# Kernel optimization log

Hardware: AMD Instinct MI355X
Metric: run time of the kernel (lower is better)

Reference implementation:

```python
import jax, jax.numpy as jnp
import numpy as np

B, M, C, D, FF, FEAT = 1, 1024, 128, 512, 1024, 20
PAIR = 3 * D + 2 * FEAT  # slow_scorer_size = 1576


def _ffnn(x, W0, b0, W1, b1):
    # FFNN(depth=1): hidden relu layer then linear output (eval mode, no dropout)
    return jax.nn.relu(x @ W0 + b0) @ W1 + b1


def _batch_gather(x, idx):
    # x: [B, M, ...], idx: [B, ...] int -> gather along mention dim per batch
    return jax.vmap(lambda xb, ib: xb[ib])(x, idx)


def _bucket_distance(d):
    # log-scale distance buckets 0..9 (identity for d<=4)
    log_idx = jnp.floor(jnp.log(jnp.maximum(d, 1).astype(jnp.float32)) / jnp.log(2.0)).astype(jnp.int32) + 3
    return jnp.clip(jnp.where(d <= 4, d, log_idx), 0, 9)


def setup_inputs() -> dict:
    key = jax.random.key(0)
    ks = jax.random.split(key, 10)
    s = 0.02
    return {
        'mention_emb': jax.random.normal(ks[0], (B, M, D), dtype=jnp.float32),
        'mention_cluster_ids': jax.random.randint(ks[1], (B, M), 0, 200),
        'mention_speaker_ids': jax.random.randint(ks[2], (B, M), 0, 2),
        'ms_W0': jax.random.normal(ks[3], (D, FF), dtype=jnp.float32) * s,
        'ms_b0': jnp.zeros((FF,), jnp.float32),
        'ms_W1': jax.random.normal(ks[4], (FF, 1), dtype=jnp.float32) * s,
        'ms_b1': jnp.zeros((1,), jnp.float32),
        'sp_W0': jax.random.normal(ks[5], (PAIR, FF), dtype=jnp.float32) * s,
        'sp_b0': jnp.zeros((FF,), jnp.float32),
        'sp_W1': jax.random.normal(ks[6], (FF, 1), dtype=jnp.float32) * s,
        'sp_b1': jnp.zeros((1,), jnp.float32),
        'speaker_emb': jax.random.normal(ks[7], (2, FEAT), dtype=jnp.float32) * s,
        'bucket_emb': jax.random.normal(ks[8], (10, FEAT), dtype=jnp.float32) * s,
    }


def reference(mention_emb, mention_cluster_ids, mention_speaker_ids,
              ms_W0, ms_b0, ms_W1, ms_b1,
              sp_W0, sp_b0, sp_W1, sp_b1,
              speaker_emb, bucket_emb):
    # mention scoring
    mention_scores = _ffnn(mention_emb, ms_W0, ms_b0, ms_W1, ms_b1)[..., 0]  # [B, M]

    # get_antecedent_info: fixed window of C previous mentions
    offsets = jnp.arange(1, C + 1)[None, None, :]                    # [1,1,C]
    raw = jnp.arange(M)[None, :, None] - offsets                      # [1,M,C]
    antecedents = jnp.broadcast_to(jnp.clip(raw, 0, M - 1), (B, M, C))
    ant_mask = jnp.broadcast_to(raw >= 0, (B, M, C))

    fast_scores = _batch_gather(mention_scores, antecedents) + mention_scores[:, :, None]
    antecedent_emb = _batch_gather(mention_emb, antecedents)          # [B,M,C,D]

    # slow pair scorer features
    same_speaker = (_batch_gather(mention_speaker_ids, antecedents) == mention_speaker_ids[:, :, None]).astype(jnp.int32)
    speaker_feat = speaker_emb[same_speaker]                          # [B,M,C,FEAT]
    bucket_feat = jnp.broadcast_to(bucket_emb[_bucket_distance(offsets)], (B, M, C, FEAT))

    src = jnp.broadcast_to(mention_emb[:, :, None, :], (B, M, C, D))
    pair_emb = jnp.concatenate([src, antecedent_emb, src * antecedent_emb, speaker_feat, bucket_feat], axis=-1)
    slow_scores = _ffnn(pair_emb, sp_W0, sp_b0, sp_W1, sp_b1)[..., 0]  # [B,M,C]

    antecedent_scores = fast_scores + slow_scores + jnp.log(ant_mask.astype(jnp.float32))
    overall_scores = jnp.concatenate([jnp.zeros((B, M, 1), jnp.float32), antecedent_scores], axis=2)
    overall_dist = jax.nn.softmax(overall_scores, axis=-1)
    eps = 1e-6
    overall_dist = jnp.clip(overall_dist, eps, 1.0 - eps)
    overall_dist = overall_dist / jnp.sum(overall_dist, axis=-1, keepdims=True)

    # coref loss from cluster ids
    ant_cluster = _batch_gather(mention_cluster_ids, antecedents) * ant_mask.astype(mention_cluster_ids.dtype)
    same_cluster = ant_cluster == mention_cluster_ids[:, :, None]
    non_dummy = (mention_cluster_ids > 0)[:, :, None]
    ant_labels = same_cluster & non_dummy
    dummy_labels = ~jnp.any(ant_labels, axis=2, keepdims=True)
    overall_labels = jnp.concatenate([dummy_labels, ant_labels], axis=2)
    loss = -jnp.sum(jnp.log(overall_dist) * overall_labels.astype(jnp.float32), axis=2)
    loss = jnp.mean(jnp.sum(loss, axis=1))
    return overall_dist, loss
```

## Files before the change

kernel.cpp:

```cpp
#include <hip/hip_runtime.h>
#include <math.h>

#define MM 1024
#define DD 512
#define CC 128
#define LDSR 516


typedef __attribute__((ext_vector_type(8))) short bf16x8;
typedef __attribute__((ext_vector_type(4), aligned(8))) short bf16x4a;
typedef __attribute__((ext_vector_type(4))) float f32x4;

__device__ __forceinline__ ushort bf16_rn(float x) {
    uint u = __float_as_uint(x);
    uint r = u + 0x7fffu + ((u >> 16) & 1u);
    return (ushort)(r >> 16);
}
__device__ __forceinline__ float bf16_to_f(ushort u) {
    return __uint_as_float(((uint)u) << 16);
}
__device__ __forceinline__ bf16x8 ld_lds16(const ushort* p) {
    bf16x4a lo = *(const bf16x4a*)p;
    bf16x4a hi = *(const bf16x4a*)(p + 4);
    return __builtin_shufflevector(lo, hi, 0, 1, 2, 3, 4, 5, 6, 7);
}

__global__ __launch_bounds__(256) void prep_emb(const float* __restrict__ emb,
                                                ushort* __restrict__ embb)
{
    int i = blockIdx.x * 256 + threadIdx.x;
    float2 v = ((const float2*)emb)[i];
    ushort2 o;
    o.x = bf16_rn(v.x);
    o.y = bf16_rn(v.y);
    ((ushort2*)embb)[i] = o;
}

__global__ __launch_bounds__(256) void prep_wall(const float* __restrict__ ms_W0,
                                                 const float* __restrict__ sp_W0,
                                                 ushort* __restrict__ Wall)
{
    __shared__ float t[64][65];
    const int k0 = blockIdx.x * 64;
    const int n0 = blockIdx.y * 64;
    const int g = n0 >> 10;
    const float* src = (g == 0) ? ms_W0 : (sp_W0 + (size_t)(g - 1) * 512 * 1024);
    const int col0 = n0 & 1023;
    const int tr = threadIdx.x >> 6, tc = threadIdx.x & 63;
#pragma unroll
    for (int i = 0; i < 16; ++i) {
        int k = tr + i * 4;
        t[k][tc] = src[(size_t)(k0 + k) * 1024 + col0 + tc];
    }
    __syncthreads();
    const int f = threadIdx.x >> 2;
    const int c4 = threadIdx.x & 3;
    ushort tmp[16];
#pragma unroll
    for (int j = 0; j < 16; ++j) tmp[j] = bf16_rn(t[c4 * 16 + j][f]);
    uint4* dst = (uint4*)(Wall + (size_t)(n0 + f) * 512 + k0 + c4 * 16);
    dst[0] = *(uint4*)&tmp[0];
    dst[1] = *(uint4*)&tmp[8];
}

__global__ __launch_bounds__(64) void prep_wfragP(const float* __restrict__ W,
                                                  ushort* __restrict__ dst_frag)
{
    const int bid = blockIdx.x;
    const int l = threadIdx.x;
    const int g2 = bid >> 5, s = (bid >> 1) & 15, j = bid & 1;
    const int wave = g2 >> 2, ft = g2 & 3;
    const int t16 = wave * 8 + ft * 2 + j;
    const int f = t16 * 16 + (l & 15);
    const int kb = s * 32 + ((l >> 4) & 3) * 8;
    ushort tmp[8];
#pragma unroll
    for (int e = 0; e < 8; ++e) tmp[e] = bf16_rn(W[(size_t)(kb + e) * 1024 + f]);
    uint4* dst = (uint4*)(dst_frag + (size_t)bid * 512 + l * 8);
    *dst = *(uint4*)&tmp[0];
}

__global__ __launch_bounds__(256) void gemm_h_mfma(
    const ushort* __restrict__ embb, const ushort* __restrict__ Wall,
    float* __restrict__ H)
{
    const int n0 = blockIdx.x * 128;
    const int m0 = blockIdx.y * 128;
    const int lane = threadIdx.x & 63, wave = threadIdx.x >> 6;
    const int wx = wave & 1, wy = wave >> 1;
    const int l15 = lane & 15, lq = lane >> 4;

    const ushort* arow[4];
#pragma unroll
    for (int mi = 0; mi < 4; ++mi)
        arow[mi] = embb + (size_t)(m0 + wy * 64 + mi * 16 + l15) * 512;
    const ushort* brow[4];
#pragma unroll
    for (int ni = 0; ni < 4; ++ni)
        brow[ni] = Wall + (size_t)(n0 + wx * 64 + ni * 16 + l15) * 512;

    f32x4 acc[4][4];
#pragma unroll
    for (int i = 0; i < 4; ++i)
#pragma unroll
        for (int j = 0; j < 4; ++j) acc[i][j] = (f32x4)0.f;

    for (int kt = 0; kt < 512; kt += 32) {
        const int ko = kt + lq * 8;
        bf16x8 av[4], bv[4];
#pragma unroll
        for (int mi = 0; mi < 4; ++mi) av[mi] = *(const bf16x8*)(arow[mi] + ko);
#pragma unroll
        for (int ni = 0; ni < 4; ++ni) bv[ni] = *(const bf16x8*)(brow[ni] + ko);
#pragma unroll
        for (int mi = 0; mi < 4; ++mi)
#pragma unroll
            for (int ni = 0; ni < 4; ++ni)
                acc[mi][ni] = __builtin_amdgcn_mfma_f32_16x16x32_bf16(av[mi], bv[ni], acc[mi][ni], 0, 0, 0);
    }
#pragma unroll
    for (int mi = 0; mi < 4; ++mi)
#pragma unroll
        for (int r = 0; r < 4; ++r) {
            int mrow = m0 + wy * 64 + mi * 16 + lq * 4 + r;
#pragma unroll
            for (int ni = 0; ni < 4; ++ni)
                H[(size_t)mrow * 3072 + n0 + wx * 64 + ni * 16 + l15] = acc[mi][ni][r];
        }
}

__global__ void small_proj(const float* __restrict__ speaker_emb,
                           const float* __restrict__ bucket_emb,
                           const float* __restrict__ sp_W0,
                           float* __restrict__ spk_proj, float* __restrict__ bkt_proj)
{
    int r = blockIdx.x;
    const float* e; const float* W; float* out;
    if (r < 2) { e = speaker_emb + r * 20; W = sp_W0 + (size_t)1536 * 1024; out = spk_proj + r * 1024; }
    else       { e = bucket_emb + (r - 2) * 20; W = sp_W0 + (size_t)1556 * 1024; out = bkt_proj + (r - 2) * 1024; }
    float ek[20];
#pragma unroll
    for (int k = 0; k < 20; ++k) ek[k] = e[k];
    for (int f = threadIdx.x; f < 1024; f += blockDim.x) {
        float s = 0.f;
#pragma unroll
        for (int k = 0; k < 20; ++k) s = fmaf(ek[k], W[(size_t)k * 1024 + f], s);
        out[f] = s;
    }
}

__global__ __launch_bounds__(256) void mention_score(
    const float* __restrict__ H, const float* __restrict__ ms_b0,
    const float* __restrict__ ms_W1, const float* __restrict__ ms_b1,
    float* __restrict__ ms)
{
    int m = blockIdx.x;
    float v = 0.f;
    for (int f = threadIdx.x; f < 1024; f += 256) {
        float h = H[(size_t)m * 3072 + f] + ms_b0[f];
        v += fmaxf(h, 0.f) * ms_W1[f];
    }
#pragma unroll
    for (int o = 1; o < 64; o <<= 1) v += __shfl_xor(v, o);
    __shared__ float sm[4];
    if ((threadIdx.x & 63) == 0) sm[threadIdx.x >> 6] = v;
    __syncthreads();
    if (threadIdx.x == 0) ms[m] = sm[0] + sm[1] + sm[2] + sm[3] + ms_b1[0];
}

__global__ __launch_bounds__(512, 8) void pair_mfma(
    const ushort* __restrict__ embb, const ushort* __restrict__ WfragP,
    const float* __restrict__ H, const float* __restrict__ spk_proj,
    const float* __restrict__ bkt_proj, const float* __restrict__ sp_b0,
    const float* __restrict__ sp_W1, const int* __restrict__ speaker,
    float* __restrict__ slow)
{
    extern __shared__ ushort Alds[];
    float* red = (float*)(Alds + 32 * LDSR);
    int* meta_ss = (int*)(red + 8 * 32);
    int* meta_bk = meta_ss + 32;
    const int m = blockIdx.x;
    const int cq = blockIdx.y;
    const int cbase = cq * 32;
    const int tid = threadIdx.x;
    const int spk_m = speaker[m];

    {
        const int c = tid & 31;
        const int kh = (tid >> 5) * 32;
        int a = m - 1 - (cbase + c); if (a < 0) a = 0;
        const ushort* ea = embb + (size_t)a * 512 + kh;
        const ushort* em = embb + (size_t)m * 512 + kh;
        ushort* dst = Alds + c * LDSR + kh;
#pragma unroll
        for (int j = 0; j < 32; j += 8) {
            bf16x8 va = *(const bf16x8*)(ea + j);
            bf16x8 vm = *(const bf16x8*)(em + j);
            uint pr[4];
#pragma unroll
            for (int p = 0; p < 4; ++p) {
                float q0 = bf16_to_f((ushort)va[2 * p])     * bf16_to_f((ushort)vm[2 * p]);
                float q1 = bf16_to_f((ushort)va[2 * p + 1]) * bf16_to_f((ushort)vm[2 * p + 1]);
                pr[p] = __builtin_amdgcn_perm(__float_as_uint(q1), __float_as_uint(q0), 0x07060302u);
            }
            *(uint2*)(dst + j)     = *(uint2*)&pr[0];
            *(uint2*)(dst + j + 4) = *(uint2*)&pr[2];
        }
        if (tid < 32) {
            meta_ss[c] = (speaker[a] == spk_m) ? 1 : 0;
            int off = cbase + c + 1;
            int bk;
            if (off <= 4) bk = off;
            else { bk = 31 - __clz(off) + 3; if (bk > 9) bk = 9; }
            meta_bk[c] = bk;
        }
    }
    __syncthreads();

    const int lane = tid & 63;
    const int wave = __builtin_amdgcn_readfirstlane(tid >> 6);
    const int l15 = lane & 15, lq = lane >> 4;
    const ushort* ab0 = Alds + l15 * LDSR + lq * 8;

    const float* Hsrc = H + m * 3072 + 1024;
    const float* Hant = H + 2048;

    float sacc[2][4];
#pragma unroll
    for (int ct = 0; ct < 2; ++ct)
#pragma unroll
        for (int r = 0; r < 4; ++r) sacc[ct][r] = 0.f;

#pragma unroll 1
    for (int ft = 0; ft < 4; ++ft) {
        const int f0a = wave * 128 + ft * 32;
        const ushort* bb = WfragP + (size_t)(wave * 4 + ft) * 16384 + (size_t)lane * 8;
        f32x4 acc[2][2];
#pragma unroll
        for (int i = 0; i < 2; ++i)
#pragma unroll
            for (int j = 0; j < 2; ++j) acc[i][j] = (f32x4)0.f;

#pragma unroll 4
        for (int s = 0; s < 16; ++s) {
            bf16x8 b0 = *(const bf16x8*)(bb + s * 1024);
            bf16x8 b1 = *(const bf16x8*)(bb + s * 1024 + 512);
            bf16x8 a0 = ld_lds16(ab0 + s * 32);
            bf16x8 a1 = ld_lds16(ab0 + 16 * LDSR + s * 32);
            __builtin_amdgcn_s_setprio(1);
            acc[0][0] = __builtin_amdgcn_mfma_f32_16x16x32_bf16(a0, b0, acc[0][0], 0, 0, 0);
            acc[0][1] = __builtin_amdgcn_mfma_f32_16x16x32_bf16(a0, b1, acc[0][1], 0, 0, 0);
            acc[1][0] = __builtin_amdgcn_mfma_f32_16x16x32_bf16(a1, b0, acc[1][0], 0, 0, 0);
            acc[1][1] = __builtin_amdgcn_mfma_f32_16x16x32_bf16(a1, b1, acc[1][1], 0, 0, 0);
            __builtin_amdgcn_s_setprio(0);
        }

        float srcb[2], w1v[2], sp0v[2], sp1v[2];
#pragma unroll
        for (int fi = 0; fi < 2; ++fi) {
            const int fcol = f0a + fi * 16 + l15;
            srcb[fi] = Hsrc[fcol] + sp_b0[fcol];
            w1v[fi]  = sp_W1[fcol];
            sp0v[fi] = spk_proj[fcol];
            sp1v[fi] = spk_proj[1024 + fcol];
        }
#pragma unroll
        for (int ct = 0; ct < 2; ++ct) {
#pragma unroll
            for (int reg = 0; reg < 4; ++reg) {
                const int cl = ct * 16 + lq * 4 + reg;
                int a = m - 1 - (cbase + cl); if (a < 0) a = 0;
                const int ss = meta_ss[cl];
                const int aidx = a * 3072;
                const int bidx = meta_bk[cl] << 10;
                float s = sacc[ct][reg];
#pragma unroll
                for (int fi = 0; fi < 2; ++fi) {
                    const int fcol = f0a + fi * 16 + l15;
                    float bval = bkt_proj[bidx + fcol];
                    float pre = acc[ct][fi][reg] + srcb[fi] + Hant[aidx + fcol]
                              + (ss ? sp1v[fi] : sp0v[fi]) + bval;
                    s += fmaxf(pre, 0.f) * w1v[fi];
                }
                sacc[ct][reg] = s;
            }
        }
    }

#pragma unroll
    for (int ct = 0; ct < 2; ++ct) {
#pragma unroll
        for (int reg = 0; reg < 4; ++reg) {
            float s = sacc[ct][reg];
            s += __shfl_xor(s, 1); s += __shfl_xor(s, 2);
            s += __shfl_xor(s, 4); s += __shfl_xor(s, 8);
            if (l15 == 0) red[wave * 32 + ct * 16 + lq * 4 + reg] = s;
        }
    }
    __syncthreads();
    if (tid < 32) {
        float s = 0.f;
#pragma unroll
        for (int i = 0; i < 8; ++i) s += red[i * 32 + tid];
        slow[m * 128 + cbase + tid] = s;
    }
}

__device__ __forceinline__ float bsum2(float v, float* sm) {
#pragma unroll
    for (int o = 1; o < 64; o <<= 1) v += __shfl_xor(v, o);
    __syncthreads();
    if ((threadIdx.x & 63) == 0) sm[threadIdx.x >> 6] = v;
    __syncthreads();
    return sm[0] + sm[1];
}
__device__ __forceinline__ float bmax2(float v, float* sm) {
#pragma unroll
    for (int o = 1; o < 64; o <<= 1) v = fmaxf(v, __shfl_xor(v, o));
    __syncthreads();
    if ((threadIdx.x & 63) == 0) sm[threadIdx.x >> 6] = v;
    __syncthreads();
    return fmaxf(sm[0], sm[1]);
}

__global__ __launch_bounds__(128) void softmax_loss(
    const float* __restrict__ slow, const float* __restrict__ ms,
    const float* __restrict__ sp_b1, const int* __restrict__ cluster,
    float* __restrict__ out, float* __restrict__ loss_partial)
{
    const int m = blockIdx.x, c = threadIdx.x;
    __shared__ float sm[2];
    const int raw = m - 1 - c;
    const bool maskv = raw >= 0;
    const int a = maskv ? raw : 0;
    float score = slow[(size_t)m * 128 + c] + sp_b1[0] + ms[m] + ms[a];
    if (!maskv) score = -INFINITY;

    float mx = fmaxf(bmax2(score, sm), 0.f);
    float e = expf(score - mx);
    float e0 = expf(0.f - mx);
    float sum = bsum2(e, sm) + e0;
    float p = e / sum, p0 = e0 / sum;
    const float eps = 1e-6f;
    p  = fminf(fmaxf(p,  eps), 1.f - eps);
    p0 = fminf(fmaxf(p0, eps), 1.f - eps);
    float sum2 = bsum2(p, sm) + p0;
    p /= sum2; p0 /= sum2;
    out[(size_t)m * 129 + 1 + c] = p;
    if (c == 0) out[(size_t)m * 129] = p0;

    const int cid = cluster[m];
    const bool lbl = maskv && (cid > 0) && (cluster[a] == cid);
    float anyc = bsum2(lbl ? 1.f : 0.f, sm);
    float lsum = bsum2(lbl ? -logf(p) : 0.f, sm);
    if (c == 0) {
        if (anyc == 0.f) lsum += -logf(p0);
        loss_partial[m] = lsum;
    }
}

__global__ void loss_sum(const float* __restrict__ lp, float* __restrict__ out) {
    float v = 0.f;
    for (int i = threadIdx.x; i < 1024; i += 256) v += lp[i];
#pragma unroll
    for (int o = 1; o < 64; o <<= 1) v += __shfl_xor(v, o);
    __shared__ float sm[4];
    if ((threadIdx.x & 63) == 0) sm[threadIdx.x >> 6] = v;
    __syncthreads();
    if (threadIdx.x == 0) out[(size_t)1024 * 129] = sm[0] + sm[1] + sm[2] + sm[3];
}

extern "C" void kernel_launch(void* const* d_in, const int* in_sizes, int n_in,
                              void* d_out, int out_size, void* d_ws, size_t ws_size,
                              hipStream_t stream)
{
    const float* emb   = (const float*)d_in[0];
    const int*   clus  = (const int*)  d_in[1];
    const int*   spk   = (const int*)  d_in[2];
    const float* ms_W0 = (const float*)d_in[3];
    const float* ms_b0 = (const float*)d_in[4];
    const float* ms_W1 = (const float*)d_in[5];
    const float* ms_b1 = (const float*)d_in[6];
    const float* sp_W0 = (const float*)d_in[7];
    const float* sp_b0 = (const float*)d_in[8];
    const float* sp_W1 = (const float*)d_in[9];
    const float* sp_b1 = (const float*)d_in[10];
    const float* spke  = (const float*)d_in[11];
    const float* bkte  = (const float*)d_in[12];

    float* ws = (float*)d_ws;
    float* H        = ws;
    float* slow     = ws + 3145728;
    float* spk_proj = ws + 3276800;
    float* bkt_proj = ws + 3278848;
    float* msc      = ws + 3289088;
    float* lossp    = ws + 3290112;
    ushort* embb    = (ushort*)(ws + 3291136);
    ushort* Wall    = (ushort*)(ws + 3553280);
    ushort* WfragP  = Wall + (size_t)3072 * 512;
    float* out = (float*)d_out;

    const int pair_lds = 32 * LDSR * 2 + 8 * 32 * 4 + 2 * 32 * 4;

    static bool attr_set = false;
    if (!attr_set) {
        hipFuncSetAttribute((const void*)&pair_mfma,
                            hipFuncAttributeMaxDynamicSharedMemorySize,
                            pair_lds);
        attr_set = true;
    }

    hipLaunchKernelGGL(prep_emb, dim3(1024), dim3(256), 0, stream, emb, embb);
    hipLaunchKernelGGL(prep_wall, dim3(8, 48), dim3(256), 0, stream, ms_W0, sp_W0, Wall);
    hipLaunchKernelGGL(prep_wfragP, dim3(1024), dim3(64), 0, stream,
                       sp_W0 + (size_t)1024 * 1024, WfragP);
    hipLaunchKernelGGL(gemm_h_mfma, dim3(24, 8), dim3(256), 0, stream, embb, Wall, H);
    hipLaunchKernelGGL(small_proj, dim3(12), dim3(256), 0, stream, spke, bkte, sp_W0, spk_proj, bkt_proj);
    hipLaunchKernelGGL(mention_score, dim3(1024), dim3(256), 0, stream, H, ms_b0, ms_W1, ms_b1, msc);
    hipLaunchKernelGGL(pair_mfma, dim3(1024, 4), dim3(512), pair_lds, stream,
                       embb, WfragP, H, spk_proj, bkt_proj, sp_b0, sp_W1, spk, slow);
    hipLaunchKernelGGL(softmax_loss, dim3(1024), dim3(128), 0, stream,
                       slow, msc, sp_b1, clus, out, lossp);
    hipLaunchKernelGGL(loss_sum, dim3(1), dim3(256), 0, stream, lossp, out);
}
```

Baseline: 347.9 us.

## Merge prep kernels into one launch and fuse mention scoring into GEMM epilogue

The four preprocessing kernels (emb cast, W transpose, fragment pack, small projections) become one kernel that dispatches on block index. Mention scoring is folded into the H GEMM epilogue: blocks covering the first 1024 columns apply bias, relu and the W1 dot product, then atomically add into the mention scores instead of writing H. The intent is fewer launches and no write-then-reread of that part of H. In exchange it adds a memset, float atomics that make summation order nondeterministic, and moves ms_b1 into softmax as 2*ms_b1.

```diff
diff --git a/kernel.cpp b/kernel.cpp
--- a/kernel.cpp
+++ b/kernel.cpp
@@ -25,64 +25,88 @@
     return __builtin_shufflevector(lo, hi, 0, 1, 2, 3, 4, 5, 6, 7);
 }
 
-__global__ __launch_bounds__(256) void prep_emb(const float* __restrict__ emb,
-                                                ushort* __restrict__ embb)
-{
-    int i = blockIdx.x * 256 + threadIdx.x;
-    float2 v = ((const float2*)emb)[i];
-    ushort2 o;
-    o.x = bf16_rn(v.x);
-    o.y = bf16_rn(v.y);
-    ((ushort2*)embb)[i] = o;
-}
-
-__global__ __launch_bounds__(256) void prep_wall(const float* __restrict__ ms_W0,
-                                                 const float* __restrict__ sp_W0,
-                                                 ushort* __restrict__ Wall)
-{
-    __shared__ float t[64][65];
-    const int k0 = blockIdx.x * 64;
-    const int n0 = blockIdx.y * 64;
-    const int g = n0 >> 10;
-    const float* src = (g == 0) ? ms_W0 : (sp_W0 + (size_t)(g - 1) * 512 * 1024);
-    const int col0 = n0 & 1023;
-    const int tr = threadIdx.x >> 6, tc = threadIdx.x & 63;
-#pragma unroll
-    for (int i = 0; i < 16; ++i) {
-        int k = tr + i * 4;
-        t[k][tc] = src[(size_t)(k0 + k) * 1024 + col0 + tc];
-    }
-    __syncthreads();
-    const int f = threadIdx.x >> 2;
-    const int c4 = threadIdx.x & 3;
-    ushort tmp[16];
-#pragma unroll
-    for (int j = 0; j < 16; ++j) tmp[j] = bf16_rn(t[c4 * 16 + j][f]);
-    uint4* dst = (uint4*)(Wall + (size_t)(n0 + f) * 512 + k0 + c4 * 16);
-    dst[0] = *(uint4*)&tmp[0];
-    dst[1] = *(uint4*)&tmp[8];
-}
-
-__global__ __launch_bounds__(64) void prep_wfragP(const float* __restrict__ W,
-                                                  ushort* __restrict__ dst_frag)
+__global__ __launch_bounds__(256) void prep_all(
+    const float* __restrict__ emb, ushort* __restrict__ embb,
+    const float* __restrict__ ms_W0, const float* __restrict__ sp_W0,
+    ushort* __restrict__ Wall, ushort* __restrict__ WfragP,
+    const float* __restrict__ speaker_emb, const float* __restrict__ bucket_emb,
+    float* __restrict__ spk_proj, float* __restrict__ bkt_proj)
 {
     const int bid = blockIdx.x;
-    const int l = threadIdx.x;
-    const int g2 = bid >> 5, s = (bid >> 1) & 15, j = bid & 1;
-    const int wave = g2 >> 2, ft = g2 & 3;
-    const int t16 = wave * 8 + ft * 2 + j;
-    const int f = t16 * 16 + (l & 15);
-    const int kb = s * 32 + ((l >> 4) & 3) * 8;
-    ushort tmp[8];
-#pragma unroll
-    for (int e = 0; e < 8; ++e) tmp[e] = bf16_rn(W[(size_t)(kb + e) * 1024 + f]);
-    uint4* dst = (uint4*)(dst_frag + (size_t)bid * 512 + l * 8);
-    *dst = *(uint4*)&tmp[0];
-}
-
-__global__ __launch_bounds__(256) void gemm_h_mfma(
+    const int tid = threadIdx.x;
+
+    if (bid < 1024) {
+        int i = bid * 256 + tid;
+        float2 v = ((const float2*)emb)[i];
+        ushort2 o;
+        o.x = bf16_rn(v.x);
+        o.y = bf16_rn(v.y);
+        ((ushort2*)embb)[i] = o;
+        return;
+    }
+    if (bid < 1408) {
+        __shared__ float t[64][65];
+        const int r = bid - 1024;
+        const int k0 = (r & 7) * 64;
+        const int n0 = (r >> 3) * 64;
+        const int g = n0 >> 10;
+        const float* src = (g == 0) ? ms_W0 : (sp_W0 + (size_t)(g - 1) * 512 * 1024);
+        const int col0 = n0 & 1023;
+        const int tr = tid >> 6, tc = tid & 63;
+#pragma unroll
+        for (int i = 0; i < 16; ++i) {
+            int k = tr + i * 4;
+            t[k][tc] = src[(size_t)(k0 + k) * 1024 + col0 + tc];
+        }
+        __syncthreads();
+        const int f = tid >> 2;
+        const int c4 = tid & 3;
+        ushort tmp[16];
+#pragma unroll
+        for (int j = 0; j < 16; ++j) tmp[j] = bf16_rn(t[c4 * 16 + j][f]);
+        uint4* dst = (uint4*)(Wall + (size_t)(n0 + f) * 512 + k0 + c4 * 16);
+        dst[0] = *(uint4*)&tmp[0];
+        dst[1] = *(uint4*)&tmp[8];
+        return;
+    }
+    if (bid < 1664) {
+        const int b4 = (bid - 1408) * 4 + (tid >> 6);
+        const int l = tid & 63;
+        const int g2 = b4 >> 5, s = (b4 >> 1) & 15, j = b4 & 1;
+        const int wv = g2 >> 2, ft = g2 & 3;
+        const int t16 = wv * 8 + ft * 2 + j;
+        const int f = t16 * 16 + (l & 15);
+        const int kb = s * 32 + ((l >> 4) & 3) * 8;
+        const float* W = sp_W0 + (size_t)1024 * 1024;
+        ushort tmp[8];
+#pragma unroll
+        for (int e = 0; e < 8; ++e) tmp[e] = bf16_rn(W[(size_t)(kb + e) * 1024 + f]);
+        uint4* dst = (uint4*)(WfragP + (size_t)b4 * 512 + l * 8);
+        *dst = *(uint4*)&tmp[0];
+        return;
+    }
+    {
+        const int r = bid - 1664;
+        const float* e; const float* W; float* out;
+        if (r < 2) { e = speaker_emb + r * 20; W = sp_W0 + (size_t)1536 * 1024; out = spk_proj + r * 1024; }
+        else       { e = bucket_emb + (r - 2) * 20; W = sp_W0 + (size_t)1556 * 1024; out = bkt_proj + (r - 2) * 1024; }
+        float ek[20];
+#pragma unroll
+        for (int k = 0; k < 20; ++k) ek[k] = e[k];
+        for (int f = tid; f < 1024; f += 256) {
+            float s = 0.f;
+#pragma unroll
+            for (int k = 0; k < 20; ++k) s = fmaf(ek[k], W[(size_t)k * 1024 + f], s);
+            out[f] = s;
+        }
+        return;
+    }
+}
+
+__global__ __launch_bounds__(256) void gemm_h_ms(
     const ushort* __restrict__ embb, const ushort* __restrict__ Wall,
-    float* __restrict__ H)
+    const float* __restrict__ ms_b0, const float* __restrict__ ms_W1,
+    float* __restrict__ H, float* __restrict__ ms)
 {
     const int n0 = blockIdx.x * 128;
     const int m0 = blockIdx.y * 128;
@@ -118,54 +142,41 @@
             for (int ni = 0; ni < 4; ++ni)
                 acc[mi][ni] = __builtin_amdgcn_mfma_f32_16x16x32_bf16(av[mi], bv[ni], acc[mi][ni], 0, 0, 0);
     }
-#pragma unroll
-    for (int mi = 0; mi < 4; ++mi)
-#pragma unroll
-        for (int r = 0; r < 4; ++r) {
-            int mrow = m0 + wy * 64 + mi * 16 + lq * 4 + r;
-#pragma unroll
-            for (int ni = 0; ni < 4; ++ni)
-                H[(size_t)mrow * 3072 + n0 + wx * 64 + ni * 16 + l15] = acc[mi][ni][r];
-        }
-}
-
-__global__ void small_proj(const float* __restrict__ speaker_emb,
-                           const float* __restrict__ bucket_emb,
-                           const float* __restrict__ sp_W0,
-                           float* __restrict__ spk_proj, float* __restrict__ bkt_proj)
-{
-    int r = blockIdx.x;
-    const float* e; const float* W; float* out;
-    if (r < 2) { e = speaker_emb + r * 20; W = sp_W0 + (size_t)1536 * 1024; out = spk_proj + r * 1024; }
-    else       { e = bucket_emb + (r - 2) * 20; W = sp_W0 + (size_t)1556 * 1024; out = bkt_proj + (r - 2) * 1024; }
-    float ek[20];
-#pragma unroll
-    for (int k = 0; k < 20; ++k) ek[k] = e[k];
-    for (int f = threadIdx.x; f < 1024; f += blockDim.x) {
-        float s = 0.f;
-#pragma unroll
-        for (int k = 0; k < 20; ++k) s = fmaf(ek[k], W[(size_t)k * 1024 + f], s);
-        out[f] = s;
-    }
-}
-
-__global__ __launch_bounds__(256) void mention_score(
-    const float* __restrict__ H, const float* __restrict__ ms_b0,
-    const float* __restrict__ ms_W1, const float* __restrict__ ms_b1,
-    float* __restrict__ ms)
-{
-    int m = blockIdx.x;
-    float v = 0.f;
-    for (int f = threadIdx.x; f < 1024; f += 256) {
-        float h = H[(size_t)m * 3072 + f] + ms_b0[f];
-        v += fmaxf(h, 0.f) * ms_W1[f];
-    }
-#pragma unroll
-    for (int o = 1; o < 64; o <<= 1) v += __shfl_xor(v, o);
-    __shared__ float sm[4];
-    if ((threadIdx.x & 63) == 0) sm[threadIdx.x >> 6] = v;
-    __syncthreads();
-    if (threadIdx.x == 0) ms[m] = sm[0] + sm[1] + sm[2] + sm[3] + ms_b1[0];
+
+    if (n0 < 1024) {
+        float b0v[4], w1v[4];
+#pragma unroll
+        for (int ni = 0; ni < 4; ++ni) {
+            const int col = n0 + wx * 64 + ni * 16 + l15;
+            b0v[ni] = ms_b0[col];
+            w1v[ni] = ms_W1[col];
+        }
+#pragma unroll
+        for (int mi = 0; mi < 4; ++mi)
+#pragma unroll
+            for (int r = 0; r < 4; ++r) {
+                float s = 0.f;
+#pragma unroll
+                for (int ni = 0; ni < 4; ++ni)
+                    s += fmaxf(acc[mi][ni][r] + b0v[ni], 0.f) * w1v[ni];
+                s += __shfl_xor(s, 1); s += __shfl_xor(s, 2);
+                s += __shfl_xor(s, 4); s += __shfl_xor(s, 8);
+                if (l15 == 0) {
+                    const int mrow = m0 + wy * 64 + mi * 16 + lq * 4 + r;
+                    atomicAdd(&ms[mrow], s);
+                }
+            }
+    } else {
+#pragma unroll
+        for (int mi = 0; mi < 4; ++mi)
+#pragma unroll
+            for (int r = 0; r < 4; ++r) {
+                int mrow = m0 + wy * 64 + mi * 16 + lq * 4 + r;
+#pragma unroll
+                for (int ni = 0; ni < 4; ++ni)
+                    H[(size_t)mrow * 3072 + n0 + wx * 64 + ni * 16 + l15] = acc[mi][ni][r];
+            }
+    }
 }
 
 __global__ __launch_bounds__(512, 8) void pair_mfma(
@@ -325,6 +336,7 @@
 
 __global__ __launch_bounds__(128) void softmax_loss(
     const float* __restrict__ slow, const float* __restrict__ ms,
+    const float* __restrict__ ms_b1,
     const float* __restrict__ sp_b1, const int* __restrict__ cluster,
     float* __restrict__ out, float* __restrict__ loss_partial)
 {
@@ -333,7 +345,8 @@
     const int raw = m - 1 - c;
     const bool maskv = raw >= 0;
     const int a = maskv ? raw : 0;
-    float score = slow[(size_t)m * 128 + c] + sp_b1[0] + ms[m] + ms[a];
+    float score = slow[(size_t)m * 128 + c] + sp_b1[0]
+                + ms[m] + ms[a] + 2.f * ms_b1[0];
     if (!maskv) score = -INFINITY;
 
     float mx = fmaxf(bmax2(score, sm), 0.f);
@@ -410,16 +423,15 @@
         attr_set = true;
     }
 
-    hipLaunchKernelGGL(prep_emb, dim3(1024), dim3(256), 0, stream, emb, embb);
-    hipLaunchKernelGGL(prep_wall, dim3(8, 48), dim3(256), 0, stream, ms_W0, sp_W0, Wall);
-    hipLaunchKernelGGL(prep_wfragP, dim3(1024), dim3(64), 0, stream,
-                       sp_W0 + (size_t)1024 * 1024, WfragP);
-    hipLaunchKernelGGL(gemm_h_mfma, dim3(24, 8), dim3(256), 0, stream, embb, Wall, H);
-    hipLaunchKernelGGL(small_proj, dim3(12), dim3(256), 0, stream, spke, bkte, sp_W0, spk_proj, bkt_proj);
-    hipLaunchKernelGGL(mention_score, dim3(1024), dim3(256), 0, stream, H, ms_b0, ms_W1, ms_b1, msc);
+    hipMemsetAsync(msc, 0, 1024 * sizeof(float), stream);
+    hipLaunchKernelGGL(prep_all, dim3(1676), dim3(256), 0, stream,
+                       emb, embb, ms_W0, sp_W0, Wall, WfragP,
+                       spke, bkte, spk_proj, bkt_proj);
+    hipLaunchKernelGGL(gemm_h_ms, dim3(24, 8), dim3(256), 0, stream,
+                       embb, Wall, ms_b0, ms_W1, H, msc);
     hipLaunchKernelGGL(pair_mfma, dim3(1024, 4), dim3(512), pair_lds, stream,
                        embb, WfragP, H, spk_proj, bkt_proj, sp_b0, sp_W1, spk, slow);
     hipLaunchKernelGGL(softmax_loss, dim3(1024), dim3(128), 0, stream,
-                       slow, msc, sp_b1, clus, out, lossp);
+                       slow, msc, ms_b1, sp_b1, clus, out, lossp);
     hipLaunchKernelGGL(loss_sum, dim3(1), dim3(256), 0, stream, lossp, out);
 }
```

Measured after the change: 329.2 us. 1.06x faster.
